# Performance work log

Hardware: AMD Instinct MI355X
Metric: run time of the kernel (lower is better)

## Reference

```python
import jax, jax.numpy as jnp
import numpy as np


def _three_nn(xyz1, xyz2):
    # xyz1: [B,N1,3], xyz2: [B,N2,3]
    # Squared euclidean distances, as in the original three_nn CUDA/TF op.
    d2 = (jnp.sum(xyz1 * xyz1, axis=-1)[:, :, None]
          + jnp.sum(xyz2 * xyz2, axis=-1)[:, None, :]
          - 2.0 * jnp.einsum('bnd,bmd->bnm', xyz1, xyz2))  # [B,N1,N2]
    neg_vals, idx = jax.lax.top_k(-d2, 3)                 # 3 smallest
    return -neg_vals, idx                                  # dist [B,N1,3], idx [B,N1,3]


def reference(xyz1, xyz2, points1, points2, w1, w2):
    dist, idx = _three_nn(xyz1, xyz2)
    dist = jnp.maximum(dist, 1e-10)
    inv = 1.0 / dist                                       # [B,N1,3]
    weight = inv / jnp.sum(inv, axis=2, keepdims=True)     # [B,N1,3]

    B = points2.shape[0]
    b_idx = jnp.arange(B)[:, None, None]
    gathered = points2[b_idx, idx]                         # [B,N1,3,C2]
    interpolated = jnp.einsum('bnk,bnkc->bnc', weight, gathered)  # [B,N1,C2]

    new_points = jnp.concatenate([interpolated, points1], axis=2)  # [B,N1,C2+C1]

    # 1x1 conv MLP = per-point matmul; bn=False, activation=relu on all layers
    h = jax.nn.relu(jnp.einsum('bnc,cf->bnf', new_points, w1))
    h = jax.nn.relu(jnp.einsum('bnc,cf->bnf', h, w2))
    return h


def setup_inputs() -> dict:
    key = jax.random.key(0)
    k1, k2, k3, k4, k5, k6 = jax.random.split(key, 6)
    B, N1, N2, C1, C2 = 4, 8192, 2048, 128, 256
    xyz1 = jax.random.normal(k1, (B, N1, 3), dtype=jnp.float32)
    xyz2 = jax.random.normal(k2, (B, N2, 3), dtype=jnp.float32)
    points1 = jax.random.normal(k3, (B, N1, C1), dtype=jnp.float32)
    points2 = jax.random.normal(k4, (B, N2, C2), dtype=jnp.float32)
    # glorot-normal-ish init for the 1x1 conv kernels
    w1 = jax.random.normal(k5, (C2 + C1, 256), dtype=jnp.float32) * (2.0 / (C2 + C1 + 256)) ** 0.5
    w2 = jax.random.normal(k6, (256, 256), dtype=jnp.float32) * (2.0 / (256 + 256)) ** 0.5
    return {"xyz1": xyz1, "xyz2": xyz2, "points1": points1, "points2": points2, "w1": w1, "w2": w2}
```

## Files before the change

kernel.cpp:

```cpp
#include <hip/hip_runtime.h>
#include <stdint.h>

typedef unsigned short u16;
typedef unsigned int   u32;

#define NB 4
#define N1 8192
#define N2 2048
#define C1 128
#define C2 256
#define KK1 384
#define FF 256
#define TM 64
#define NTHR 1024
#define NCH 16
#define CHSZ (N2 / NCH)
#define TILES_PER_B (N1 / TM)
#define APAD 400
#define HPAD 272
#define NKT1 (KK1 / 32)
#define NKT2 (FF / 32)
#define ABYTES (TM * APAD * 2)
#define PDOFF  ABYTES
#define PIOFF  (ABYTES + NCH * TM * 3 * 4)

typedef short short8 __attribute__((ext_vector_type(8)));
typedef float floatx4 __attribute__((ext_vector_type(4)));
typedef float f32x2  __attribute__((ext_vector_type(2)));
typedef u32   u32x4  __attribute__((ext_vector_type(4)));

union ABFrag { u32 u[4]; short8 v; u32x4 q; };

__device__ __forceinline__ u16 f2b(float f) {
    u32 x = __float_as_uint(f);
    return (u16)((x + 0x7FFFu + ((x >> 16) & 1u)) >> 16);
}
__device__ __forceinline__ u32 pack2(float a, float b) {
    return (u32)f2b(a) | ((u32)f2b(b) << 16);
}

__global__ __launch_bounds__(256) void prep_kernel(
    const float* __restrict__ w1, const float* __restrict__ w2,
    const float* __restrict__ xyz2,
    u32x4* __restrict__ w1F, u32x4* __restrict__ w2F, float* __restrict__ xq)
{
    int i = blockIdx.x * 256 + threadIdx.x;
    if (i < 16 * NKT1 * 64) {
        int nt = i / (NKT1 * 64), rem = i % (NKT1 * 64);
        int kt = rem / 64, lane = rem % 64;
        int n  = nt * 16 + (lane & 15);
        int k0 = kt * 32 + (lane >> 4) * 8;
        const float* wc = w1 + n;
        ABFrag f;
        f.u[0] = pack2(wc[(k0 + 0) * FF], wc[(k0 + 1) * FF]);
        f.u[1] = pack2(wc[(k0 + 2) * FF], wc[(k0 + 3) * FF]);
        f.u[2] = pack2(wc[(k0 + 4) * FF], wc[(k0 + 5) * FF]);
        f.u[3] = pack2(wc[(k0 + 6) * FF], wc[(k0 + 7) * FF]);
        w1F[i] = f.q;
        return;
    }
    i -= 16 * NKT1 * 64;
    if (i < 16 * NKT2 * 64) {
        int nt = i / (NKT2 * 64), rem = i % (NKT2 * 64);
        int kt = rem / 64, lane = rem % 64;
        int n  = nt * 16 + (lane & 15);
        int k0 = kt * 32 + (lane >> 4) * 8;
        const float* wc = w2 + n;
        ABFrag f;
        f.u[0] = pack2(wc[(k0 + 0) * FF], wc[(k0 + 1) * FF]);
        f.u[1] = pack2(wc[(k0 + 2) * FF], wc[(k0 + 3) * FF]);
        f.u[2] = pack2(wc[(k0 + 4) * FF], wc[(k0 + 5) * FF]);
        f.u[3] = pack2(wc[(k0 + 6) * FF], wc[(k0 + 7) * FF]);
        w2F[i] = f.q;
        return;
    }
    i -= 16 * NKT2 * 64;
    if (i < NB * N2) {
        const float* q = xyz2 + (size_t)i * 3;
        float x = q[0], y = q[1], z = q[2];
        float s2 = __fadd_rn(__fadd_rn(__fmul_rn(x,x), __fmul_rn(y,y)), __fmul_rn(z,z));
        int p = i >> 1, e = i & 1;
        float* rec = xq + (size_t)p * 8;
        rec[0 + e] = -2.0f * x;
        rec[2 + e] = -2.0f * y;
        rec[4 + e] = -2.0f * z;
        rec[6 + e] = s2;
    }
}

__global__ __launch_bounds__(NTHR, 8) void fp_fused_kernel(
    const float* __restrict__ xyz1, const float* __restrict__ p1,
    const float* __restrict__ p2,
    const u32x4* __restrict__ w1F,  const u32x4* __restrict__ w2F,
    const float4* __restrict__ xq,  float* __restrict__ out)
{
    __shared__ int   s_idx[TM][3];
    __shared__ float s_wt[TM][3];
    __shared__ __align__(16) char s_buf[ABYTES + NCH * TM * 3 * 8];

    const int tid = threadIdx.x;
    const int b   = blockIdx.x / TILES_PER_B;
    const int t0  = (blockIdx.x % TILES_PER_B) * TM;

    u16*   A  = (u16*)s_buf;
    float* pd = (float*)(s_buf + PDOFF);
    int*   pi = (int*)(s_buf + PIOFF);

    {
        const int c4 = (tid & 31) * 4, r32 = tid >> 5;
        #pragma unroll
        for (int rv = 0; rv < 2; ++rv) {
            int rr = r32 + rv * 32;
            float4 v = *(const float4*)(p1 + ((size_t)b * N1 + t0 + rr) * C1 + c4);
            u32* w = (u32*)(A + rr * APAD + 256 + c4);
            w[0] = pack2(v.x, v.y);
            w[1] = pack2(v.z, v.w);
        }
    }

    {
        const int r  = tid & 63;
        const int ch = __builtin_amdgcn_readfirstlane(tid >> 6);
        const float4* cb = xq + ((size_t)b * (N2 / 2) + ch * (CHSZ / 2)) * 2;
        const float* q = xyz1 + ((size_t)b * N1 + t0 + r) * 3;
        float qx = q[0], qy = q[1], qz = q[2];
        float s1 = __fadd_rn(__fadd_rn(__fmul_rn(qx,qx), __fmul_rn(qy,qy)), __fmul_rn(qz,qz));
        float bd0 = 3e38f, bd1 = 3e38f, bd2 = 3e38f;
        int   bi0 = 0, bi1 = 0, bi2 = 0;
        const int j0 = ch * CHSZ;
        #pragma unroll 4
        for (int jj = 0; jj < CHSZ / 2; ++jj) {
            float4 f0 = cb[2 * jj];
            float4 f1 = cb[2 * jj + 1];
            f32x2 dpair;
            {
                #pragma clang fp contract(off)
                f32x2 qx2 = {qx, qx}, qy2 = {qy, qy}, qz2 = {qz, qz}, s1v = {s1, s1};
                f32x2 nx = {f0.x, f0.y}, ny = {f0.z, f0.w};
                f32x2 nz = {f1.x, f1.y}, ss = {f1.z, f1.w};
                f32x2 u  = qx2 * nx;
                f32x2 v  = qy2 * ny;
                f32x2 w  = u + v;
                f32x2 z2 = qz2 * nz;
                f32x2 t  = w + z2;
                f32x2 s12 = s1v + ss;
                dpair = s12 + t;
            }
            #pragma unroll
            for (int e = 0; e < 2; ++e) {
                float d = dpair[e];
                int   j = j0 + 2 * jj + e;
                float nb0 = fminf(d, bd0);
                float nb1 = __builtin_amdgcn_fmed3f(d, bd0, bd1);
                float nb2 = __builtin_amdgcn_fmed3f(d, bd1, bd2);
                bool c0 = d < bd0, c1 = d < bd1, c2 = d < bd2;
                int t01 = c0 ? bi0 : j;
                bi0     = c0 ? j   : bi0;
                int t12 = c1 ? bi1 : j;
                bi1     = c1 ? t01 : bi1;
                bi2     = c2 ? t12 : bi2;
                bd0 = nb0; bd1 = nb1; bd2 = nb2;
            }
        }
        const int o = (ch * TM + r) * 3;
        pd[o+0] = bd0; pd[o+1] = bd1; pd[o+2] = bd2;
        pi[o+0] = bi0; pi[o+1] = bi1; pi[o+2] = bi2;
    }
    __syncthreads();

    if (tid < TM) {
        float d0 = 3e38f, d1 = 3e38f, d2 = 3e38f;
        int   i0 = 0, i1 = 0, i2 = 0;
        for (int c = 0; c < NCH; ++c) {
            const int o = (c * TM + tid) * 3;
            #pragma unroll
            for (int k = 0; k < 3; ++k) {
                float d = pd[o + k]; int ix = pi[o + k];
                float n0 = fminf(d, d0);
                float n1 = __builtin_amdgcn_fmed3f(d, d0, d1);
                float n2 = __builtin_amdgcn_fmed3f(d, d1, d2);
                bool c0 = d < d0, c1 = d < d1, c2 = d < d2;
                int t01 = c0 ? i0 : ix;
                i0      = c0 ? ix : i0;
                int t12 = c1 ? i1 : t01;
                i1      = c1 ? t01 : i1;
                i2      = c2 ? t12 : i2;
                d0 = n0; d1 = n1; d2 = n2;
            }
        }
        d0 = fmaxf(d0, 1e-10f); d1 = fmaxf(d1, 1e-10f); d2 = fmaxf(d2, 1e-10f);
        float v0 = 1.0f / d0, v1 = 1.0f / d1, v2 = 1.0f / d2;
        float s  = 1.0f / (v0 + v1 + v2);
        s_wt[tid][0] = v0 * s; s_wt[tid][1] = v1 * s; s_wt[tid][2] = v2 * s;
        s_idx[tid][0] = i0; s_idx[tid][1] = i1; s_idx[tid][2] = i2;
    }
    __syncthreads();

    {
        const float* pb = p2 + (size_t)b * N2 * C2;
        const int col4 = (tid & 63) * 4;
        const int wvr  = tid >> 6;
        #pragma unroll
        for (int m = 0; m < 4; ++m) {
            int rr = wvr + m * 16;
            float w0 = s_wt[rr][0], w1v = s_wt[rr][1], w2v = s_wt[rr][2];
            int   i0 = s_idx[rr][0], i1 = s_idx[rr][1], i2 = s_idx[rr][2];
            float4 a0 = *(const float4*)(pb + (size_t)i0 * C2 + col4);
            float4 a1 = *(const float4*)(pb + (size_t)i1 * C2 + col4);
            float4 a2 = *(const float4*)(pb + (size_t)i2 * C2 + col4);
            float e0 = w0 * a0.x + w1v * a1.x + w2v * a2.x;
            float e1 = w0 * a0.y + w1v * a1.y + w2v * a2.y;
            float e2 = w0 * a0.z + w1v * a1.z + w2v * a2.z;
            float e3 = w0 * a0.w + w1v * a1.w + w2v * a2.w;
            u32* w = (u32*)(A + rr * APAD + col4);
            w[0] = pack2(e0, e1);
            w[1] = pack2(e2, e3);
        }
    }
    __syncthreads();

    const int lane = tid & 63;
    const int wv   = tid >> 6;
    const int lr   = lane & 15;
    const int lg   = lane >> 4;
    const int wvb  = wv * 16;

    int id1[4], id2[4];
    {
        u16 rbf = f2b((float)lr);
        u16 c32 = f2b(1.0f / 32.0f);
        ABFrag pa, pc;
        u32 ra = (u32)rbf | ((u32)rbf << 16);
        u32 rc = (u32)c32 | ((u32)c32 << 16);
        pa.u[0] = pa.u[1] = pa.u[2] = pa.u[3] = ra;
        pc.u[0] = pc.u[1] = pc.u[2] = pc.u[3] = rc;
        floatx4 z = {0.f, 0.f, 0.f, 0.f};
        floatx4 D1 = __builtin_amdgcn_mfma_f32_16x16x32_bf16(pa.v, pc.v, z, 0, 0, 0);
        floatx4 D2 = __builtin_amdgcn_mfma_f32_16x16x32_bf16(pc.v, pa.v, z, 0, 0, 0);
        #pragma unroll
        for (int g = 0; g < 4; ++g) { id1[g] = (int)(D1[g] + 0.5f); id2[g] = (int)(D2[g] + 0.5f); }
    }

    floatx4 acc[4];
    #pragma unroll
    for (int i = 0; i < 4; ++i) acc[i] = floatx4{0.f, 0.f, 0.f, 0.f};

    {
        const u32x4* wf = w1F + (size_t)(wv * NKT1) * 64 + lane;
        const int kb8 = lg * 8;
        for (int kk = 0; kk < NKT1; ++kk) {
            ABFrag bf; bf.q = wf[(size_t)kk * 64];
            ABFrag a[4];
            #pragma unroll
            for (int rt = 0; rt < 4; ++rt)
                a[rt].q = *(const u32x4*)(A + (rt * 16 + lr) * APAD + kk * 32 + kb8);
            #pragma unroll
            for (int rt = 0; rt < 4; ++rt)
                acc[rt] = __builtin_amdgcn_mfma_f32_16x16x32_bf16(a[rt].v, bf.v, acc[rt], 0, 0, 0);
        }
    }
    __syncthreads();

    u16* H = (u16*)s_buf;
    #pragma unroll
    for (int rt = 0; rt < 4; ++rt)
        #pragma unroll
        for (int g = 0; g < 4; ++g) {
            int row = rt * 16 + id1[g];
            int col = wvb + id2[g];
            H[row * HPAD + col] = f2b(fmaxf(acc[rt][g], 0.0f));
        }
    __syncthreads();

    floatx4 acc2[4];
    #pragma unroll
    for (int i = 0; i < 4; ++i) acc2[i] = floatx4{0.f, 0.f, 0.f, 0.f};

    {
        const u32x4* wf = w2F + (size_t)(wv * NKT2) * 64 + lane;
        const int kb8 = lg * 8;
        for (int kk = 0; kk < NKT2; ++kk) {
            ABFrag bf; bf.q = wf[(size_t)kk * 64];
            ABFrag a[4];
            #pragma unroll
            for (int rt = 0; rt < 4; ++rt)
                a[rt].q = *(const u32x4*)(H + (rt * 16 + lr) * HPAD + kk * 32 + kb8);
            #pragma unroll
            for (int rt = 0; rt < 4; ++rt)
                acc2[rt] = __builtin_amdgcn_mfma_f32_16x16x32_bf16(a[rt].v, bf.v, acc2[rt], 0, 0, 0);
        }
    }

    float* ob = out + ((size_t)b * N1 + t0) * FF;
    #pragma unroll
    for (int rt = 0; rt < 4; ++rt)
        #pragma unroll
        for (int g = 0; g < 4; ++g) {
            int row = rt * 16 + id1[g];
            int col = wvb + id2[g];
            ob[(size_t)row * FF + col] = fmaxf(acc2[rt][g], 0.0f);
        }
}

extern "C" void kernel_launch(void* const* d_in, const int* in_sizes, int n_in,
                              void* d_out, int out_size, void* d_ws, size_t ws_size,
                              hipStream_t stream)
{
    (void)in_sizes; (void)n_in; (void)out_size; (void)ws_size;
    const float* xyz1 = (const float*)d_in[0];
    const float* xyz2 = (const float*)d_in[1];
    const float* p1   = (const float*)d_in[2];
    const float* p2   = (const float*)d_in[3];
    const float* w1   = (const float*)d_in[4];
    const float* w2   = (const float*)d_in[5];
    float* out = (float*)d_out;

    u32x4* w1F = (u32x4*)d_ws;
    u32x4* w2F = w1F + 16 * NKT1 * 64;
    float* xqw = (float*)(w2F + 16 * NKT2 * 64);

    int prep_items = 16 * NKT1 * 64 + 16 * NKT2 * 64 + NB * N2;
    prep_kernel<<<(prep_items + 255) / 256, 256, 0, stream>>>(w1, w2, xyz2, w1F, w2F, xqw);
    fp_fused_kernel<<<NB * TILES_PER_B, NTHR, 0, stream>>>(
        xyz1, p1, p2, w1F, w2F, (const float4*)xqw, out);
}
```

Before: 62.75 us.

## Split kNN search into separate partial kernel, stash partials in output buffer

Moves the three-nearest-neighbour search out of the fused GEMM kernel into its own kernel. It runs 4x as many 256-thread blocks, each scanning a quarter of the reference points, and writes partial top-3 results into unused tail columns of the output buffer. The GEMM kernel then merges the four partials before interpolation and the MLP. This frees shared memory and occupancy in the GEMM kernel and gives the search more parallelism, at the cost of an extra launch and global round-trips. bf16 packing also switches to the hardware v_cvt_pk_bf16_f32 instruction.

Result: slower. 66.44 us (+5.9%).

```diff
diff --git a/kernel.cpp b/kernel.cpp
--- a/kernel.cpp
+++ b/kernel.cpp
@@ -12,17 +12,13 @@
 #define KK1 384
 #define FF 256
 #define TM 64
-#define NTHR 1024
-#define NCH 16
-#define CHSZ (N2 / NCH)
 #define TILES_PER_B (N1 / TM)
 #define APAD 400
 #define HPAD 272
 #define NKT1 (KK1 / 32)
 #define NKT2 (FF / 32)
-#define ABYTES (TM * APAD * 2)
-#define PDOFF  ABYTES
-#define PIOFF  (ABYTES + NCH * TM * 3 * 4)
+#define QPTS 512
+#define RECF 232
 
 typedef short short8 __attribute__((ext_vector_type(8)));
 typedef float floatx4 __attribute__((ext_vector_type(4)));
@@ -36,7 +32,9 @@
     return (u16)((x + 0x7FFFu + ((x >> 16) & 1u)) >> 16);
 }
 __device__ __forceinline__ u32 pack2(float a, float b) {
-    return (u32)f2b(a) | ((u32)f2b(b) << 16);
+    u32 r;
+    asm("v_cvt_pk_bf16_f32 %0, %1, %2" : "=v"(r) : "v"(a), "v"(b));
+    return r;
 }
 
 __global__ __launch_bounds__(256) void prep_kernel(
@@ -88,48 +86,31 @@
     }
 }
 
-__global__ __launch_bounds__(NTHR, 8) void fp_fused_kernel(
-    const float* __restrict__ xyz1, const float* __restrict__ p1,
-    const float* __restrict__ p2,
-    const u32x4* __restrict__ w1F,  const u32x4* __restrict__ w2F,
-    const float4* __restrict__ xq,  float* __restrict__ out)
+__global__ __launch_bounds__(256, 8) void knn_part_kernel(
+    const float* __restrict__ xyz1, const float4* __restrict__ xq,
+    float* __restrict__ out)
 {
-    __shared__ int   s_idx[TM][3];
-    __shared__ float s_wt[TM][3];
-    __shared__ __align__(16) char s_buf[ABYTES + NCH * TM * 3 * 8];
-
-    const int tid = threadIdx.x;
-    const int b   = blockIdx.x / TILES_PER_B;
-    const int t0  = (blockIdx.x % TILES_PER_B) * TM;
-
-    u16*   A  = (u16*)s_buf;
-    float* pd = (float*)(s_buf + PDOFF);
-    int*   pi = (int*)(s_buf + PIOFF);
-
-    {
-        const int c4 = (tid & 31) * 4, r32 = tid >> 5;
-        #pragma unroll
-        for (int rv = 0; rv < 2; ++rv) {
-            int rr = r32 + rv * 32;
-            float4 v = *(const float4*)(p1 + ((size_t)b * N1 + t0 + rr) * C1 + c4);
-            u32* w = (u32*)(A + rr * APAD + 256 + c4);
-            w[0] = pack2(v.x, v.y);
-            w[1] = pack2(v.z, v.w);
-        }
-    }
-
-    {
-        const int r  = tid & 63;
-        const int ch = __builtin_amdgcn_readfirstlane(tid >> 6);
-        const float4* cb = xq + ((size_t)b * (N2 / 2) + ch * (CHSZ / 2)) * 2;
+    __shared__ float pd[4][TM][3];
+    __shared__ int   pi[4][TM][3];
+
+    const int tid  = threadIdx.x;
+    const int bq   = blockIdx.x & 3;
+    const int tile = (blockIdx.x >> 2) & (TILES_PER_B - 1);
+    const int b    = blockIdx.x >> 9;
+    const int t0   = tile * TM;
+    const int r    = tid & 63;
+    const int w    = __builtin_amdgcn_readfirstlane(tid >> 6);
+
+    {
+        const int p0 = QPTS * bq + 128 * w;
+        const float4* cb = xq + ((size_t)b * (N2 / 2) + p0 / 2) * 2;
         const float* q = xyz1 + ((size_t)b * N1 + t0 + r) * 3;
         float qx = q[0], qy = q[1], qz = q[2];
         float s1 = __fadd_rn(__fadd_rn(__fmul_rn(qx,qx), __fmul_rn(qy,qy)), __fmul_rn(qz,qz));
         float bd0 = 3e38f, bd1 = 3e38f, bd2 = 3e38f;
-        int   bi0 = 0, bi1 = 0, bi2 = 0;
-        const int j0 = ch * CHSZ;
-        #pragma unroll 4
-        for (int jj = 0; jj < CHSZ / 2; ++jj) {
+        int   bi0 = -1, bi1 = -1, bi2 = -1;
+        #pragma unroll 8
+        for (int jj = 0; jj < 64; ++jj) {
             float4 f0 = cb[2 * jj];
             float4 f1 = cb[2 * jj + 1];
             f32x2 dpair;
@@ -140,16 +121,16 @@
                 f32x2 nz = {f1.x, f1.y}, ss = {f1.z, f1.w};
                 f32x2 u  = qx2 * nx;
                 f32x2 v  = qy2 * ny;
-                f32x2 w  = u + v;
+                f32x2 ww = u + v;
                 f32x2 z2 = qz2 * nz;
-                f32x2 t  = w + z2;
+                f32x2 t  = ww + z2;
                 f32x2 s12 = s1v + ss;
                 dpair = s12 + t;
             }
             #pragma unroll
             for (int e = 0; e < 2; ++e) {
                 float d = dpair[e];
-                int   j = j0 + 2 * jj + e;
+                int   j = p0 + 2 * jj + e;
                 float nb0 = fminf(d, bd0);
                 float nb1 = __builtin_amdgcn_fmed3f(d, bd0, bd1);
                 float nb2 = __builtin_amdgcn_fmed3f(d, bd1, bd2);
@@ -162,20 +143,76 @@
                 bd0 = nb0; bd1 = nb1; bd2 = nb2;
             }
         }
-        const int o = (ch * TM + r) * 3;
-        pd[o+0] = bd0; pd[o+1] = bd1; pd[o+2] = bd2;
-        pi[o+0] = bi0; pi[o+1] = bi1; pi[o+2] = bi2;
+        pd[w][r][0] = bd0; pd[w][r][1] = bd1; pd[w][r][2] = bd2;
+        pi[w][r][0] = bi0; pi[w][r][1] = bi1; pi[w][r][2] = bi2;
     }
     __syncthreads();
 
     if (tid < TM) {
         float d0 = 3e38f, d1 = 3e38f, d2 = 3e38f;
-        int   i0 = 0, i1 = 0, i2 = 0;
-        for (int c = 0; c < NCH; ++c) {
-            const int o = (c * TM + tid) * 3;
+        int   i0 = -1, i1 = -1, i2 = -1;
+        for (int c = 0; c < 4; ++c) {
             #pragma unroll
             for (int k = 0; k < 3; ++k) {
-                float d = pd[o + k]; int ix = pi[o + k];
+                float d = pd[c][tid][k]; int ix = pi[c][tid][k];
+                float n0 = fminf(d, d0);
+                float n1 = __builtin_amdgcn_fmed3f(d, d0, d1);
+                float n2 = __builtin_amdgcn_fmed3f(d, d1, d2);
+                bool c0 = d < d0, c1 = d < d1, c2 = d < d2;
+                int t01 = c0 ? i0 : ix;
+                i0      = c0 ? ix : i0;
+                int t12 = c1 ? i1 : t01;
+                i1      = c1 ? t01 : i1;
+                i2      = c2 ? t12 : i2;
+                d0 = n0; d1 = n1; d2 = n2;
+            }
+        }
+        float* rp = out + ((size_t)(b * N1 + t0 + tid) * FF + RECF + 6 * bq);
+        *(float2*)(rp)     = make_float2(d0, d1);
+        *(float2*)(rp + 2) = make_float2(d2, __int_as_float(i0));
+        *(float2*)(rp + 4) = make_float2(__int_as_float(i1), __int_as_float(i2));
+    }
+}
+
+__global__ __launch_bounds__(1024, 8) void fp_gemm_kernel(
+    const float* __restrict__ p1, const float* __restrict__ p2,
+    const u32x4* __restrict__ w1F, const u32x4* __restrict__ w2F,
+    float* __restrict__ out)
+{
+    __shared__ int   s_idx[TM][3];
+    __shared__ float s_wt[TM][3];
+    __shared__ __align__(16) char s_buf[TM * APAD * 2];
+
+    const int tid = threadIdx.x;
+    const int b   = blockIdx.x / TILES_PER_B;
+    const int t0  = (blockIdx.x % TILES_PER_B) * TM;
+    u16* A = (u16*)s_buf;
+
+    {
+        const int c4 = (tid & 31) * 4, r32 = tid >> 5;
+        #pragma unroll
+        for (int rv = 0; rv < 2; ++rv) {
+            int rr = r32 + rv * 32;
+            float4 v = *(const float4*)(p1 + ((size_t)b * N1 + t0 + rr) * C1 + c4);
+            u32* w = (u32*)(A + rr * APAD + 256 + c4);
+            w[0] = pack2(v.x, v.y);
+            w[1] = pack2(v.z, v.w);
+        }
+    }
+
+    if (tid < TM) {
+        const float* rp = out + ((size_t)(b * N1 + t0 + tid) * FF + RECF);
+        float arr[24];
+        #pragma unroll
+        for (int v = 0; v < 6; ++v)
+            *(float4*)(arr + 4 * v) = *(const float4*)(rp + 4 * v);
+        float d0 = 3e38f, d1 = 3e38f, d2 = 3e38f;
+        int   i0 = -1, i1 = -1, i2 = -1;
+        #pragma unroll
+        for (int c = 0; c < 4; ++c) {
+            #pragma unroll
+            for (int k = 0; k < 3; ++k) {
+                float d = arr[6 * c + k]; int ix = __float_as_int(arr[6 * c + 3 + k]);
                 float n0 = fminf(d, d0);
                 float n1 = __builtin_amdgcn_fmed3f(d, d0, d1);
                 float n2 = __builtin_amdgcn_fmed3f(d, d1, d2);
@@ -223,6 +260,7 @@
     const int wv   = tid >> 6;
     const int lr   = lane & 15;
     const int lg   = lane >> 4;
+    const int kb8  = lg * 8;
     const int wvb  = wv * 16;
 
     int id1[4], id2[4];
@@ -244,10 +282,8 @@
     floatx4 acc[4];
     #pragma unroll
     for (int i = 0; i < 4; ++i) acc[i] = floatx4{0.f, 0.f, 0.f, 0.f};
-
     {
         const u32x4* wf = w1F + (size_t)(wv * NKT1) * 64 + lane;
-        const int kb8 = lg * 8;
         for (int kk = 0; kk < NKT1; ++kk) {
             ABFrag bf; bf.q = wf[(size_t)kk * 64];
             ABFrag a[4];
@@ -275,10 +311,8 @@
     floatx4 acc2[4];
     #pragma unroll
     for (int i = 0; i < 4; ++i) acc2[i] = floatx4{0.f, 0.f, 0.f, 0.f};
-
     {
         const u32x4* wf = w2F + (size_t)(wv * NKT2) * 64 + lane;
-        const int kb8 = lg * 8;
         for (int kk = 0; kk < NKT2; ++kk) {
             ABFrag bf; bf.q = wf[(size_t)kk * 64];
             ABFrag a[4];
@@ -321,6 +355,6 @@
 
     int prep_items = 16 * NKT1 * 64 + 16 * NKT2 * 64 + NB * N2;
     prep_kernel<<<(prep_items + 255) / 256, 256, 0, stream>>>(w1, w2, xyz2, w1F, w2F, xqw);
-    fp_fused_kernel<<<NB * TILES_PER_B, NTHR, 0, stream>>>(
-        xyz1, p1, p2, w1F, w2F, (const float4*)xqw, out);
-}
+    knn_part_kernel<<<NB * TILES_PER_B * 4, 256, 0, stream>>>(xyz1, (const float4*)xqw, out);
+    fp_gemm_kernel<<<NB * TILES_PER_B, 1024, 0, stream>>>(p1, p2, w1F, w2F, out);
+}
```
